# Kernel tuning notes

Measured on AMD Instinct MI355X. Metric: run time of the kernel, lower is better.

## Reference

```python
import jax, jax.numpy as jnp
import numpy as np

B, T, I, H = 256, 2048, 128, 128

def setup_inputs() -> dict:
    key = jax.random.key(0)
    k = jax.random.split(key, 5)
    bound = 1.0 / np.sqrt(H)  # torch RNNCell init: U(-1/sqrt(H), 1/sqrt(H))
    return {
        "x": jax.random.normal(k[0], (B, T, I), dtype=jnp.float32),
        "weight_ih": jax.random.uniform(k[1], (H, I), jnp.float32, -bound, bound),
        "weight_hh": jax.random.uniform(k[2], (H, H), jnp.float32, -bound, bound),
        "bias_ih": jax.random.uniform(k[3], (H,), jnp.float32, -bound, bound),
        "bias_hh": jax.random.uniform(k[4], (H,), jnp.float32, -bound, bound),
    }

def reference(x, weight_ih, weight_hh, bias_ih, bias_hh):
    # Tanh RNN: h_t = tanh(x_t @ W_ih^T + b_ih + h_{t-1} @ W_hh^T + b_hh)
    # Precompute the input projection for all timesteps (one big GEMM),
    # then scan the recurrent part (sequential dependency on h).
    b = x.shape[0]
    h0 = jnp.zeros((b, weight_hh.shape[0]), dtype=x.dtype)
    # [B, T, H]
    x_proj = jnp.einsum('bti,hi->bth', x, weight_ih) + bias_ih + bias_hh

    def step(h, xt):  # xt: [B, H]
        h_new = jnp.tanh(xt + h @ weight_hh.T)
        return h_new, h_new

    _, out = jax.lax.scan(step, h0, jnp.swapaxes(x_proj, 0, 1))  # out: [T, B, H]
    return jnp.swapaxes(out, 0, 1)  # [B, T, H]
```

## Files before the change

kernel.cpp:

```cpp
#include <hip/hip_runtime.h>

#define BB 256
#define TT 2048
#define II 128
#define HH 128
#define GS 16
#define NG (TT / GS)

typedef __attribute__((ext_vector_type(8))) short short8;
typedef __attribute__((ext_vector_type(4))) float f32x4;

__device__ __forceinline__ void step_barrier() {
    asm volatile("s_waitcnt lgkmcnt(0)\n\ts_barrier" ::: "memory");
}

__device__ __forceinline__ float tanh_fast(float s) {
#if __has_builtin(__builtin_amdgcn_exp2f)
    const float e = __builtin_amdgcn_exp2f(s * 2.8853900817779268f);
#else
    const float e = exp2f(s * 2.8853900817779268f);
#endif
    return 1.0f - 2.0f * __builtin_amdgcn_rcpf(e + 1.0f);
}

__device__ __forceinline__ unsigned int f2bf(float f) {
    unsigned int u = __float_as_uint(f);
    u += 0x7FFF + ((u >> 16) & 1);
    return u >> 16;
}
__device__ __forceinline__ unsigned int pack2(float lo, float hi) {
    return f2bf(lo) | (f2bf(hi) << 16);
}

__launch_bounds__(512, 1)
__global__ void rnn_pipe(const float* __restrict__ x,
                         const float* __restrict__ w_ih,
                         const float* __restrict__ w_hh,
                         const float* __restrict__ b_ih,
                         const float* __restrict__ b_hh,
                         float* __restrict__ out) {
    const int b    = blockIdx.x;
    const int tid  = threadIdx.x;
    const int wave = tid >> 6;
    const int lane = tid & 63;
    const bool hw  = (wave < 4);

    __shared__ __align__(16) unsigned short hA[2][HH];
    __shared__ __align__(16) float axbuf[3][GS][HH];
    __shared__ __align__(16) unsigned short xstage[2][4][64][8];

    const float* xb = x + (size_t)b * (TT * II);
    const f32x4 z4 = {0.f, 0.f, 0.f, 0.f};

    const int jb_h = (wave & 3) * 32;
    short8 WH[2][4];
    if (hw) {
#pragma unroll
        for (int nt = 0; nt < 2; ++nt) {
            const int jj = jb_h + nt * 16 + (lane & 15);
#pragma unroll
            for (int kf = 0; kf < 4; ++kf) {
                short8 s;
#pragma unroll
                for (int e = 0; e < 8; ++e) {
                    const int kp = kf * 32 + (lane >> 4) * 8 + e;
                    const int mm = kp & 31;
                    const int ko = (kp & ~31) + (mm >> 1) + ((mm & 1) << 4);
                    s[e] = (short)f2bf(w_hh[(size_t)jj * HH + ko]);
                }
                WH[nt][kf] = s;
            }
        }
    }

    const int xwq = wave - 4;
    const int jb  = xwq * 32;
    short8 WF[2][4];
    float biasv[2];
    f32x4 bs0 = z4, bs1 = z4;
    const int q   = tid - 256;
    const int t_s = q >> 4;
    const int m   = q & 15;
    const int i0  = m * 8;
    const int kfs = m >> 2;
    const int lps = (m & 3) * 16 + t_s;
    if (!hw) {
#pragma unroll
        for (int nt = 0; nt < 2; ++nt) {
            const int jj = jb + nt * 16 + (lane & 15);
            biasv[nt] = b_ih[jj] + b_hh[jj];
#pragma unroll
            for (int kf = 0; kf < 4; ++kf) {
                const float* wp = w_ih + (size_t)jj * II + kf * 32 + (lane >> 4) * 8;
                short8 s;
#pragma unroll
                for (int e = 0; e < 8; ++e) s[e] = (short)f2bf(wp[e]);
                WF[nt][kf] = s;
            }
        }
#pragma unroll
        for (int r = 0; r < 4; ++r) { bs0[r] = biasv[0]; bs1[r] = biasv[1]; }
    }

#define STAGE_X(BUF, R0, R1) do { \
        uint4 P_; P_.x = pack2((R0).x, (R0).y); P_.y = pack2((R0).z, (R0).w); \
        P_.z = pack2((R1).x, (R1).y); P_.w = pack2((R1).z, (R1).w); \
        *reinterpret_cast<uint4*>(&xstage[BUF][kfs][lps][0]) = P_; } while (0)

#define XPROJ(SB, AB) do { \
        const short8 PA0 = *reinterpret_cast<const short8*>(&xstage[SB][0][lane][0]); \
        const short8 PA1 = *reinterpret_cast<const short8*>(&xstage[SB][1][lane][0]); \
        const short8 PA2 = *reinterpret_cast<const short8*>(&xstage[SB][2][lane][0]); \
        const short8 PA3 = *reinterpret_cast<const short8*>(&xstage[SB][3][lane][0]); \
        f32x4 ac0 = z4, ac1 = z4; \
        ac0 = __builtin_amdgcn_mfma_f32_16x16x32_bf16(PA0, WF[0][0], ac0, 0, 0, 0); \
        ac0 = __builtin_amdgcn_mfma_f32_16x16x32_bf16(PA1, WF[0][1], ac0, 0, 0, 0); \
        ac0 = __builtin_amdgcn_mfma_f32_16x16x32_bf16(PA2, WF[0][2], ac0, 0, 0, 0); \
        ac0 = __builtin_amdgcn_mfma_f32_16x16x32_bf16(PA3, WF[0][3], ac0, 0, 0, 0); \
        ac1 = __builtin_amdgcn_mfma_f32_16x16x32_bf16(PA0, WF[1][0], ac1, 0, 0, 0); \
        ac1 = __builtin_amdgcn_mfma_f32_16x16x32_bf16(PA1, WF[1][1], ac1, 0, 0, 0); \
        ac1 = __builtin_amdgcn_mfma_f32_16x16x32_bf16(PA2, WF[1][2], ac1, 0, 0, 0); \
        ac1 = __builtin_amdgcn_mfma_f32_16x16x32_bf16(PA3, WF[1][3], ac1, 0, 0, 0); \
        const int c_ = lane & 15, rb_ = (lane >> 4) * 4; \
        _Pragma("unroll") \
        for (int r = 0; r < 4; ++r) { \
            axbuf[AB][rb_ + r][jb + c_]      = ac0[r] + biasv[0]; \
            axbuf[AB][rb_ + r][jb + 16 + c_] = ac1[r] + biasv[1]; \
        } } while (0)

    float4 nr0, nr1;
    if (!hw) {
        float4 p0 = *reinterpret_cast<const float4*>(&xb[t_s * II + i0]);
        float4 p1 = *reinterpret_cast<const float4*>(&xb[t_s * II + i0 + 4]);
        STAGE_X(0, p0, p1);
    }
    if (tid < HH) hA[0][tid] = 0;
    __syncthreads();
    if (!hw) XPROJ(0, 0);
    __syncthreads();
    if (!hw) {
        float4 p0 = *reinterpret_cast<const float4*>(&xb[(GS + t_s) * II + i0]);
        float4 p1 = *reinterpret_cast<const float4*>(&xb[(GS + t_s) * II + i0 + 4]);
        STAGE_X(0, p0, p1);
    }
    __syncthreads();
    if (!hw) XPROJ(0, 1);
    __syncthreads();
    if (!hw) {
        float4 p0 = *reinterpret_cast<const float4*>(&xb[(2 * GS + t_s) * II + i0]);
        float4 p1 = *reinterpret_cast<const float4*>(&xb[(2 * GS + t_s) * II + i0 + 4]);
        STAGE_X(0, p0, p1);
        nr0 = *reinterpret_cast<const float4*>(&xb[(size_t)(3 * GS + t_s) * II + i0]);
        nr1 = *reinterpret_cast<const float4*>(&xb[(size_t)(3 * GS + t_s) * II + i0 + 4]);
    }
    __syncthreads();

    const int c16 = lane & 15;
    float axn0 = 0.f, axn1 = 0.f;
    f32x4 d00 = z4, d10 = z4;
    float* ob = out + (size_t)b * (TT * HH) + jb_h + lane;
    if (hw) {
        axn0 = axbuf[0][0][jb_h + c16];
        axn1 = axbuf[0][0][jb_h + 16 + c16];
    }

    for (int g = 0; g < NG; ++g) {
        const int g3  = g % 3;
        const int g3n = (g + 1) % 3;
        const int g3x = (g + 2) % 3;
#pragma unroll
        for (int w = 0; w < GS; ++w) {
            if (hw) {
                const int p  = w & 1;
                const int ko = (lane >> 4) * 8;
                const short8 A0 = *reinterpret_cast<const short8*>(&hA[p][ 0 + ko]);
                const short8 A1 = *reinterpret_cast<const short8*>(&hA[p][32 + ko]);
                const short8 A2 = *reinterpret_cast<const short8*>(&hA[p][64 + ko]);
                const short8 A3 = *reinterpret_cast<const short8*>(&hA[p][96 + ko]);
                d00[0] = axn0;
                d10[0] = axn1;
                f32x4 e01, e02, e03, e11, e12, e13;
                d00 = __builtin_amdgcn_mfma_f32_16x16x32_bf16(A0, WH[0][0], d00, 0, 0, 0);
                e01 = __builtin_amdgcn_mfma_f32_16x16x32_bf16(A1, WH[0][1], z4,  0, 0, 0);
                e02 = __builtin_amdgcn_mfma_f32_16x16x32_bf16(A2, WH[0][2], z4,  0, 0, 0);
                e03 = __builtin_amdgcn_mfma_f32_16x16x32_bf16(A3, WH[0][3], z4,  0, 0, 0);
                d10 = __builtin_amdgcn_mfma_f32_16x16x32_bf16(A0, WH[1][0], d10, 0, 0, 0);
                e11 = __builtin_amdgcn_mfma_f32_16x16x32_bf16(A1, WH[1][1], z4,  0, 0, 0);
                e12 = __builtin_amdgcn_mfma_f32_16x16x32_bf16(A2, WH[1][2], z4,  0, 0, 0);
                e13 = __builtin_amdgcn_mfma_f32_16x16x32_bf16(A3, WH[1][3], z4,  0, 0, 0);
                {
                    const int wn  = (w + 1) & (GS - 1);
                    const int gnb = (w == GS - 1) ? g3n : g3;
                    axn0 = axbuf[gnb][wn][jb_h + c16];
                    axn1 = axbuf[gnb][wn][jb_h + 16 + c16];
                }
                const float s0 = (d00[0] + e01[0]) + (e02[0] + e03[0]);
                const float s1 = (d10[0] + e11[0]) + (e12[0] + e13[0]);
                const float hn0 = tanh_fast(s0);
                const float hn1 = tanh_fast(s1);
                if (lane < 16) {
                    *reinterpret_cast<unsigned int*>(&hA[p ^ 1][jb_h + 2 * lane])
                        = pack2(hn0, hn1);
                    ob[0]  = hn0;
                    ob[16] = hn1;
                }
                ob += HH;
            } else if (w == 14) {
                if (g + 2 < NG) {
                    const short8 XA0 = *reinterpret_cast<const short8*>(&xstage[g & 1][0][lane][0]);
                    const short8 XA1 = *reinterpret_cast<const short8*>(&xstage[g & 1][1][lane][0]);
                    const short8 XA2 = *reinterpret_cast<const short8*>(&xstage[g & 1][2][lane][0]);
                    const short8 XA3 = *reinterpret_cast<const short8*>(&xstage[g & 1][3][lane][0]);
                    f32x4 xp0, xp1, xp2, xp3, yp0, yp1, yp2, yp3;
                    xp0 = __builtin_amdgcn_mfma_f32_16x16x32_bf16(XA0, WF[0][0], bs0, 0, 0, 0);
                    yp0 = __builtin_amdgcn_mfma_f32_16x16x32_bf16(XA0, WF[1][0], bs1, 0, 0, 0);
                    xp1 = __builtin_amdgcn_mfma_f32_16x16x32_bf16(XA1, WF[0][1], z4, 0, 0, 0);
                    yp1 = __builtin_amdgcn_mfma_f32_16x16x32_bf16(XA1, WF[1][1], z4, 0, 0, 0);
                    xp2 = __builtin_amdgcn_mfma_f32_16x16x32_bf16(XA2, WF[0][2], z4, 0, 0, 0);
                    yp2 = __builtin_amdgcn_mfma_f32_16x16x32_bf16(XA2, WF[1][2], z4, 0, 0, 0);
                    xp3 = __builtin_amdgcn_mfma_f32_16x16x32_bf16(XA3, WF[0][3], z4, 0, 0, 0);
                    yp3 = __builtin_amdgcn_mfma_f32_16x16x32_bf16(XA3, WF[1][3], z4, 0, 0, 0);
                    const f32x4 t0 = (xp0 + xp1) + (xp2 + xp3);
                    const f32x4 t1 = (yp0 + yp1) + (yp2 + yp3);
                    const int c_ = lane & 15, rb_ = (lane >> 4) * 4;
#pragma unroll
                    for (int r = 0; r < 4; ++r) {
                        axbuf[g3x][rb_ + r][jb + c_]      = t0[r];
                        axbuf[g3x][rb_ + r][jb + 16 + c_] = t1[r];
                    }
                }
                if (g + 3 < NG) {
                    STAGE_X((g + 1) & 1, nr0, nr1);
                }
                if (g + 4 < NG) {
                    const int tb = (g + 4) * GS;
                    nr0 = *reinterpret_cast<const float4*>(&xb[(size_t)(tb + t_s) * II + i0]);
                    nr1 = *reinterpret_cast<const float4*>(&xb[(size_t)(tb + t_s) * II + i0 + 4]);
                }
            }
            step_barrier();
        }
    }
#undef XPROJ
#undef STAGE_X
}

extern "C" void kernel_launch(void* const* d_in, const int* in_sizes, int n_in,
                              void* d_out, int out_size, void* d_ws, size_t ws_size,
                              hipStream_t stream) {
    const float* x    = (const float*)d_in[0];
    const float* w_ih = (const float*)d_in[1];
    const float* w_hh = (const float*)d_in[2];
    const float* b_ih = (const float*)d_in[3];
    const float* b_hh = (const float*)d_in[4];
    float* out = (float*)d_out;

    rnn_pipe<<<BB, 512, 0, stream>>>(x, w_ih, w_hh, b_ih, b_hh, out);
}
```

Before: 502.6 us.

## Offload output stores to projection waves and use hardware bf16 packing

Global output stores move off the latency-critical recurrent waves. The input-projection waves now read the previous step's bf16-packed hidden state from LDS and write it to global memory one step behind. The bf16 packing becomes a single v_cvt_pk_bf16_f32 instruction, and the recurrent waves get raised scheduling priority with s_setprio. The trade-off is that the output is now bf16-rounded rather than full fp32 tanh values, which reduces accuracy.

```diff
diff --git a/kernel.cpp b/kernel.cpp
--- a/kernel.cpp
+++ b/kernel.cpp
@@ -28,8 +28,10 @@
     u += 0x7FFF + ((u >> 16) & 1);
     return u >> 16;
 }
-__device__ __forceinline__ unsigned int pack2(float lo, float hi) {
-    return f2bf(lo) | (f2bf(hi) << 16);
+__device__ __forceinline__ unsigned int cvtpk(float a, float b) {
+    unsigned int r;
+    asm("v_cvt_pk_bf16_f32 %0, %1, %2" : "=v"(r) : "v"(a), "v"(b));
+    return r;
 }
 
 __launch_bounds__(512, 1)
@@ -84,6 +86,7 @@
     const int i0  = m * 8;
     const int kfs = m >> 2;
     const int lps = (m & 3) * 16 + t_s;
+    const int c16 = lane & 15;
     if (!hw) {
 #pragma unroll
         for (int nt = 0; nt < 2; ++nt) {
@@ -103,8 +106,9 @@
     }
 
 #define STAGE_X(BUF, R0, R1) do { \
-        uint4 P_; P_.x = pack2((R0).x, (R0).y); P_.y = pack2((R0).z, (R0).w); \
-        P_.z = pack2((R1).x, (R1).y); P_.w = pack2((R1).z, (R1).w); \
+        uint4 P_; \
+        P_.x = cvtpk((R0).x, (R0).y); P_.y = cvtpk((R0).z, (R0).w); \
+        P_.z = cvtpk((R1).x, (R1).y); P_.w = cvtpk((R1).z, (R1).w); \
         *reinterpret_cast<uint4*>(&xstage[BUF][kfs][lps][0]) = P_; } while (0)
 
 #define XPROJ(SB, AB) do { \
@@ -155,13 +159,17 @@
     }
     __syncthreads();
 
-    const int c16 = lane & 15;
     float axn0 = 0.f, axn1 = 0.f;
     f32x4 d00 = z4, d10 = z4;
-    float* ob = out + (size_t)b * (TT * HH) + jb_h + lane;
     if (hw) {
         axn0 = axbuf[0][0][jb_h + c16];
         axn1 = axbuf[0][0][jb_h + 16 + c16];
+        __builtin_amdgcn_s_setprio(1);
+    }
+
+    float* xout = nullptr;
+    if (!hw && lane < 32) {
+        xout = out + (size_t)b * (TT * HH) + jb + c16 + ((lane & 16) ? 16 : 0);
     }
 
     for (int g = 0; g < NG; ++g) {
@@ -198,48 +206,61 @@
                 const float s1 = (d10[0] + e11[0]) + (e12[0] + e13[0]);
                 const float hn0 = tanh_fast(s0);
                 const float hn1 = tanh_fast(s1);
+                const unsigned int hpk = cvtpk(hn0, hn1);
                 if (lane < 16) {
-                    *reinterpret_cast<unsigned int*>(&hA[p ^ 1][jb_h + 2 * lane])
-                        = pack2(hn0, hn1);
-                    ob[0]  = hn0;
-                    ob[16] = hn1;
-                }
-                ob += HH;
-            } else if (w == 14) {
-                if (g + 2 < NG) {
-                    const short8 XA0 = *reinterpret_cast<const short8*>(&xstage[g & 1][0][lane][0]);
-                    const short8 XA1 = *reinterpret_cast<const short8*>(&xstage[g & 1][1][lane][0]);
-                    const short8 XA2 = *reinterpret_cast<const short8*>(&xstage[g & 1][2][lane][0]);
-                    const short8 XA3 = *reinterpret_cast<const short8*>(&xstage[g & 1][3][lane][0]);
-                    f32x4 xp0, xp1, xp2, xp3, yp0, yp1, yp2, yp3;
-                    xp0 = __builtin_amdgcn_mfma_f32_16x16x32_bf16(XA0, WF[0][0], bs0, 0, 0, 0);
-                    yp0 = __builtin_amdgcn_mfma_f32_16x16x32_bf16(XA0, WF[1][0], bs1, 0, 0, 0);
-                    xp1 = __builtin_amdgcn_mfma_f32_16x16x32_bf16(XA1, WF[0][1], z4, 0, 0, 0);
-                    yp1 = __builtin_amdgcn_mfma_f32_16x16x32_bf16(XA1, WF[1][1], z4, 0, 0, 0);
-                    xp2 = __builtin_amdgcn_mfma_f32_16x16x32_bf16(XA2, WF[0][2], z4, 0, 0, 0);
-                    yp2 = __builtin_amdgcn_mfma_f32_16x16x32_bf16(XA2, WF[1][2], z4, 0, 0, 0);
-                    xp3 = __builtin_amdgcn_mfma_f32_16x16x32_bf16(XA3, WF[0][3], z4, 0, 0, 0);
-                    yp3 = __builtin_amdgcn_mfma_f32_16x16x32_bf16(XA3, WF[1][3], z4, 0, 0, 0);
-                    const f32x4 t0 = (xp0 + xp1) + (xp2 + xp3);
-                    const f32x4 t1 = (yp0 + yp1) + (yp2 + yp3);
-                    const int c_ = lane & 15, rb_ = (lane >> 4) * 4;
-#pragma unroll
-                    for (int r = 0; r < 4; ++r) {
-                        axbuf[g3x][rb_ + r][jb + c_]      = t0[r];
-                        axbuf[g3x][rb_ + r][jb + 16 + c_] = t1[r];
+                    *reinterpret_cast<unsigned int*>(&hA[p ^ 1][jb_h + 2 * lane]) = hpk;
+                }
+            } else {
+                const int T = (g << 4) + w;
+                if (T != 0 && lane < 32) {
+                    const unsigned int rd = *reinterpret_cast<const unsigned int*>(
+                        &hA[w & 1][jb + 2 * c16]);
+                    const unsigned int v = (lane & 16) ? (rd & 0xffff0000u) : (rd << 16);
+                    xout[(size_t)(T - 1) * HH] = __uint_as_float(v);
+                }
+                if (w == 14) {
+                    if (g + 2 < NG) {
+                        const short8 XA0 = *reinterpret_cast<const short8*>(&xstage[g & 1][0][lane][0]);
+                        const short8 XA1 = *reinterpret_cast<const short8*>(&xstage[g & 1][1][lane][0]);
+                        const short8 XA2 = *reinterpret_cast<const short8*>(&xstage[g & 1][2][lane][0]);
+                        const short8 XA3 = *reinterpret_cast<const short8*>(&xstage[g & 1][3][lane][0]);
+                        f32x4 xp0, xp1, xp2, xp3, yp0, yp1, yp2, yp3;
+                        xp0 = __builtin_amdgcn_mfma_f32_16x16x32_bf16(XA0, WF[0][0], bs0, 0, 0, 0);
+                        yp0 = __builtin_amdgcn_mfma_f32_16x16x32_bf16(XA0, WF[1][0], bs1, 0, 0, 0);
+                        xp1 = __builtin_amdgcn_mfma_f32_16x16x32_bf16(XA1, WF[0][1], z4, 0, 0, 0);
+                        yp1 = __builtin_amdgcn_mfma_f32_16x16x32_bf16(XA1, WF[1][1], z4, 0, 0, 0);
+                        xp2 = __builtin_amdgcn_mfma_f32_16x16x32_bf16(XA2, WF[0][2], z4, 0, 0, 0);
+                        yp2 = __builtin_amdgcn_mfma_f32_16x16x32_bf16(XA2, WF[1][2], z4, 0, 0, 0);
+                        xp3 = __builtin_amdgcn_mfma_f32_16x16x32_bf16(XA3, WF[0][3], z4, 0, 0, 0);
+                        yp3 = __builtin_amdgcn_mfma_f32_16x16x32_bf16(XA3, WF[1][3], z4, 0, 0, 0);
+                        const f32x4 t0 = (xp0 + xp1) + (xp2 + xp3);
+                        const f32x4 t1 = (yp0 + yp1) + (yp2 + yp3);
+                        const int c_ = lane & 15, rb_ = (lane >> 4) * 4;
+#pragma unroll
+                        for (int r = 0; r < 4; ++r) {
+                            axbuf[g3x][rb_ + r][jb + c_]      = t0[r];
+                            axbuf[g3x][rb_ + r][jb + 16 + c_] = t1[r];
+                        }
                     }
-                }
-                if (g + 3 < NG) {
-                    STAGE_X((g + 1) & 1, nr0, nr1);
-                }
-                if (g + 4 < NG) {
-                    const int tb = (g + 4) * GS;
-                    nr0 = *reinterpret_cast<const float4*>(&xb[(size_t)(tb + t_s) * II + i0]);
-                    nr1 = *reinterpret_cast<const float4*>(&xb[(size_t)(tb + t_s) * II + i0 + 4]);
+                    if (g + 3 < NG) {
+                        STAGE_X((g + 1) & 1, nr0, nr1);
+                    }
+                    if (g + 4 < NG) {
+                        const int tb = (g + 4) * GS;
+                        nr0 = *reinterpret_cast<const float4*>(&xb[(size_t)(tb + t_s) * II + i0]);
+                        nr1 = *reinterpret_cast<const float4*>(&xb[(size_t)(tb + t_s) * II + i0 + 4]);
+                    }
                 }
             }
             step_barrier();
         }
+    }
+
+    if (!hw && lane < 32) {
+        const unsigned int rd = *reinterpret_cast<const unsigned int*>(
+            &hA[0][jb + 2 * c16]);
+        const unsigned int v = (lane & 16) ? (rd & 0xffff0000u) : (rd << 16);
+        xout[(size_t)(TT - 1) * HH] = __uint_as_float(v);
     }
 #undef XPROJ
 #undef STAGE_X
```

After: 464.7 us (median of 3 runs). 7.5% less time.

## Run recurrence in a single wave to drop per-step block barriers

Applied to the files above, without the earlier changes.

One wave now computes all 128 hidden units per timestep with 32 MFMAs, using weight fragments kept in registers. Because the hidden state no longer crosses waves, the per-timestep block-wide barrier is replaced by one barrier per 16-step group, synchronising only with the four input-projection waves. The block shrinks from 512 to 320 threads, and bf16 packing uses the hardware v_cvt_pk_bf16_f32 instruction. The trade-off is a longer serial MFMA chain per step on a single wave, with more register pressure from 32 weight fragments.

```diff
diff --git a/kernel.cpp b/kernel.cpp
--- a/kernel.cpp
+++ b/kernel.cpp
@@ -10,7 +10,7 @@
 typedef __attribute__((ext_vector_type(8))) short short8;
 typedef __attribute__((ext_vector_type(4))) float f32x4;
 
-__device__ __forceinline__ void step_barrier() {
+__device__ __forceinline__ void group_barrier() {
     asm volatile("s_waitcnt lgkmcnt(0)\n\ts_barrier" ::: "memory");
 }
 
@@ -28,11 +28,13 @@
     u += 0x7FFF + ((u >> 16) & 1);
     return u >> 16;
 }
-__device__ __forceinline__ unsigned int pack2(float lo, float hi) {
-    return f2bf(lo) | (f2bf(hi) << 16);
-}
-
-__launch_bounds__(512, 1)
+__device__ __forceinline__ unsigned int cvtpk(float a, float b) {
+    unsigned int r;
+    asm("v_cvt_pk_bf16_f32 %0, %1, %2" : "=v"(r) : "v"(a), "v"(b));
+    return r;
+}
+
+__launch_bounds__(320, 1)
 __global__ void rnn_pipe(const float* __restrict__ x,
                          const float* __restrict__ w_ih,
                          const float* __restrict__ w_hh,
@@ -43,7 +45,7 @@
     const int tid  = threadIdx.x;
     const int wave = tid >> 6;
     const int lane = tid & 63;
-    const bool hw  = (wave < 4);
+    const bool hw  = (wave == 0);
 
     __shared__ __align__(16) unsigned short hA[2][HH];
     __shared__ __align__(16) float axbuf[3][GS][HH];
@@ -51,34 +53,30 @@
 
     const float* xb = x + (size_t)b * (TT * II);
     const f32x4 z4 = {0.f, 0.f, 0.f, 0.f};
-
-    const int jb_h = (wave & 3) * 32;
-    short8 WH[2][4];
+    const int c16 = lane & 15;
+    const int rg  = lane >> 4;
+
+    short8 WH[8][4];
     if (hw) {
 #pragma unroll
-        for (int nt = 0; nt < 2; ++nt) {
-            const int jj = jb_h + nt * 16 + (lane & 15);
+        for (int nt = 0; nt < 8; ++nt) {
+            const int jj = nt * 16 + c16;
 #pragma unroll
             for (int kf = 0; kf < 4; ++kf) {
+                const float* wp = w_hh + (size_t)jj * HH + kf * 32 + rg * 8;
                 short8 s;
 #pragma unroll
-                for (int e = 0; e < 8; ++e) {
-                    const int kp = kf * 32 + (lane >> 4) * 8 + e;
-                    const int mm = kp & 31;
-                    const int ko = (kp & ~31) + (mm >> 1) + ((mm & 1) << 4);
-                    s[e] = (short)f2bf(w_hh[(size_t)jj * HH + ko]);
-                }
+                for (int e = 0; e < 8; ++e) s[e] = (short)f2bf(wp[e]);
                 WH[nt][kf] = s;
             }
         }
     }
 
-    const int xwq = wave - 4;
+    const int xwq = wave - 1;
     const int jb  = xwq * 32;
     short8 WF[2][4];
     float biasv[2];
-    f32x4 bs0 = z4, bs1 = z4;
-    const int q   = tid - 256;
+    const int q   = tid - 64;
     const int t_s = q >> 4;
     const int m   = q & 15;
     const int i0  = m * 8;
@@ -87,24 +85,23 @@
     if (!hw) {
 #pragma unroll
         for (int nt = 0; nt < 2; ++nt) {
-            const int jj = jb + nt * 16 + (lane & 15);
+            const int jj = jb + nt * 16 + c16;
             biasv[nt] = b_ih[jj] + b_hh[jj];
 #pragma unroll
             for (int kf = 0; kf < 4; ++kf) {
-                const float* wp = w_ih + (size_t)jj * II + kf * 32 + (lane >> 4) * 8;
+                const float* wp = w_ih + (size_t)jj * II + kf * 32 + rg * 8;
                 short8 s;
 #pragma unroll
                 for (int e = 0; e < 8; ++e) s[e] = (short)f2bf(wp[e]);
                 WF[nt][kf] = s;
             }
         }
-#pragma unroll
-        for (int r = 0; r < 4; ++r) { bs0[r] = biasv[0]; bs1[r] = biasv[1]; }
     }
 
 #define STAGE_X(BUF, R0, R1) do { \
-        uint4 P_; P_.x = pack2((R0).x, (R0).y); P_.y = pack2((R0).z, (R0).w); \
-        P_.z = pack2((R1).x, (R1).y); P_.w = pack2((R1).z, (R1).w); \
+        uint4 P_; \
+        P_.x = cvtpk((R0).x, (R0).y); P_.y = cvtpk((R0).z, (R0).w); \
+        P_.z = cvtpk((R1).x, (R1).y); P_.w = cvtpk((R1).z, (R1).w); \
         *reinterpret_cast<uint4*>(&xstage[BUF][kfs][lps][0]) = P_; } while (0)
 
 #define XPROJ(SB, AB) do { \
@@ -121,11 +118,11 @@
         ac1 = __builtin_amdgcn_mfma_f32_16x16x32_bf16(PA1, WF[1][1], ac1, 0, 0, 0); \
         ac1 = __builtin_amdgcn_mfma_f32_16x16x32_bf16(PA2, WF[1][2], ac1, 0, 0, 0); \
         ac1 = __builtin_amdgcn_mfma_f32_16x16x32_bf16(PA3, WF[1][3], ac1, 0, 0, 0); \
-        const int c_ = lane & 15, rb_ = (lane >> 4) * 4; \
+        const int rb_ = rg * 4; \
         _Pragma("unroll") \
         for (int r = 0; r < 4; ++r) { \
-            axbuf[AB][rb_ + r][jb + c_]      = ac0[r] + biasv[0]; \
-            axbuf[AB][rb_ + r][jb + 16 + c_] = ac1[r] + biasv[1]; \
+            axbuf[AB][rb_ + r][jb + c16]      = ac0[r] + biasv[0]; \
+            axbuf[AB][rb_ + r][jb + 16 + c16] = ac1[r] + biasv[1]; \
         } } while (0)
 
     float4 nr0, nr1;
@@ -134,7 +131,7 @@
         float4 p1 = *reinterpret_cast<const float4*>(&xb[t_s * II + i0 + 4]);
         STAGE_X(0, p0, p1);
     }
-    if (tid < HH) hA[0][tid] = 0;
+    if (tid < 2 * HH) ((unsigned short*)hA)[tid] = 0;
     __syncthreads();
     if (!hw) XPROJ(0, 0);
     __syncthreads();
@@ -155,90 +152,69 @@
     }
     __syncthreads();
 
-    const int c16 = lane & 15;
-    float axn0 = 0.f, axn1 = 0.f;
-    f32x4 d00 = z4, d10 = z4;
-    float* ob = out + (size_t)b * (TT * HH) + jb_h + lane;
     if (hw) {
-        axn0 = axbuf[0][0][jb_h + c16];
-        axn1 = axbuf[0][0][jb_h + 16 + c16];
-    }
-
-    for (int g = 0; g < NG; ++g) {
-        const int g3  = g % 3;
-        const int g3n = (g + 1) % 3;
-        const int g3x = (g + 2) % 3;
-#pragma unroll
-        for (int w = 0; w < GS; ++w) {
-            if (hw) {
+        __builtin_amdgcn_s_setprio(1);
+        float* op = out + (size_t)b * (TT * HH) + lane;
+        f32x4 d0 = z4, d1 = z4, d2 = z4, d3 = z4, d4 = z4, d5 = z4, d6 = z4, d7 = z4;
+
+        for (int g = 0; g < NG; ++g) {
+            const float* axg = &axbuf[g % 3][0][0];
+#pragma unroll 4
+            for (int w = 0; w < GS; ++w) {
                 const int p  = w & 1;
-                const int ko = (lane >> 4) * 8;
+                const int ko = rg * 8;
                 const short8 A0 = *reinterpret_cast<const short8*>(&hA[p][ 0 + ko]);
                 const short8 A1 = *reinterpret_cast<const short8*>(&hA[p][32 + ko]);
                 const short8 A2 = *reinterpret_cast<const short8*>(&hA[p][64 + ko]);
                 const short8 A3 = *reinterpret_cast<const short8*>(&hA[p][96 + ko]);
-                d00[0] = axn0;
-                d10[0] = axn1;
-                f32x4 e01, e02, e03, e11, e12, e13;
-                d00 = __builtin_amdgcn_mfma_f32_16x16x32_bf16(A0, WH[0][0], d00, 0, 0, 0);
-                e01 = __builtin_amdgcn_mfma_f32_16x16x32_bf16(A1, WH[0][1], z4,  0, 0, 0);
-                e02 = __builtin_amdgcn_mfma_f32_16x16x32_bf16(A2, WH[0][2], z4,  0, 0, 0);
-                e03 = __builtin_amdgcn_mfma_f32_16x16x32_bf16(A3, WH[0][3], z4,  0, 0, 0);
-                d10 = __builtin_amdgcn_mfma_f32_16x16x32_bf16(A0, WH[1][0], d10, 0, 0, 0);
-                e11 = __builtin_amdgcn_mfma_f32_16x16x32_bf16(A1, WH[1][1], z4,  0, 0, 0);
-                e12 = __builtin_amdgcn_mfma_f32_16x16x32_bf16(A2, WH[1][2], z4,  0, 0, 0);
-                e13 = __builtin_amdgcn_mfma_f32_16x16x32_bf16(A3, WH[1][3], z4,  0, 0, 0);
-                {
-                    const int wn  = (w + 1) & (GS - 1);
-                    const int gnb = (w == GS - 1) ? g3n : g3;
-                    axn0 = axbuf[gnb][wn][jb_h + c16];
-                    axn1 = axbuf[gnb][wn][jb_h + 16 + c16];
-                }
-                const float s0 = (d00[0] + e01[0]) + (e02[0] + e03[0]);
-                const float s1 = (d10[0] + e11[0]) + (e12[0] + e13[0]);
+                const float ax0 = axg[w * HH + lane];
+                const float ax1 = axg[w * HH + lane + 64];
+                d0[0] = ax0; d1[0] = ax0; d2[0] = ax0; d3[0] = ax0;
+                d4[0] = ax1; d5[0] = ax1; d6[0] = ax1; d7[0] = ax1;
+#define HR(Ak, kf) \
+                d0 = __builtin_amdgcn_mfma_f32_16x16x32_bf16(Ak, WH[0][kf], d0, 0, 0, 0); \
+                d1 = __builtin_amdgcn_mfma_f32_16x16x32_bf16(Ak, WH[1][kf], d1, 0, 0, 0); \
+                d2 = __builtin_amdgcn_mfma_f32_16x16x32_bf16(Ak, WH[2][kf], d2, 0, 0, 0); \
+                d3 = __builtin_amdgcn_mfma_f32_16x16x32_bf16(Ak, WH[3][kf], d3, 0, 0, 0); \
+                d4 = __builtin_amdgcn_mfma_f32_16x16x32_bf16(Ak, WH[4][kf], d4, 0, 0, 0); \
+                d5 = __builtin_amdgcn_mfma_f32_16x16x32_bf16(Ak, WH[5][kf], d5, 0, 0, 0); \
+                d6 = __builtin_amdgcn_mfma_f32_16x16x32_bf16(Ak, WH[6][kf], d6, 0, 0, 0); \
+                d7 = __builtin_amdgcn_mfma_f32_16x16x32_bf16(Ak, WH[7][kf], d7, 0, 0, 0);
+                HR(A0, 0) HR(A1, 1) HR(A2, 2) HR(A3, 3)
+#undef HR
+                float s0 = d0[0];
+                s0 = (rg == 1) ? d1[0] : s0;
+                s0 = (rg == 2) ? d2[0] : s0;
+                s0 = (rg == 3) ? d3[0] : s0;
+                float s1 = d4[0];
+                s1 = (rg == 1) ? d5[0] : s1;
+                s1 = (rg == 2) ? d6[0] : s1;
+                s1 = (rg == 3) ? d7[0] : s1;
                 const float hn0 = tanh_fast(s0);
                 const float hn1 = tanh_fast(s1);
-                if (lane < 16) {
-                    *reinterpret_cast<unsigned int*>(&hA[p ^ 1][jb_h + 2 * lane])
-                        = pack2(hn0, hn1);
-                    ob[0]  = hn0;
-                    ob[16] = hn1;
-                }
-                ob += HH;
-            } else if (w == 14) {
-                if (g + 2 < NG) {
-                    const short8 XA0 = *reinterpret_cast<const short8*>(&xstage[g & 1][0][lane][0]);
-                    const short8 XA1 = *reinterpret_cast<const short8*>(&xstage[g & 1][1][lane][0]);
-                    const short8 XA2 = *reinterpret_cast<const short8*>(&xstage[g & 1][2][lane][0]);
-                    const short8 XA3 = *reinterpret_cast<const short8*>(&xstage[g & 1][3][lane][0]);
-                    f32x4 xp0, xp1, xp2, xp3, yp0, yp1, yp2, yp3;
-                    xp0 = __builtin_amdgcn_mfma_f32_16x16x32_bf16(XA0, WF[0][0], bs0, 0, 0, 0);
-                    yp0 = __builtin_amdgcn_mfma_f32_16x16x32_bf16(XA0, WF[1][0], bs1, 0, 0, 0);
-                    xp1 = __builtin_amdgcn_mfma_f32_16x16x32_bf16(XA1, WF[0][1], z4, 0, 0, 0);
-                    yp1 = __builtin_amdgcn_mfma_f32_16x16x32_bf16(XA1, WF[1][1], z4, 0, 0, 0);
-                    xp2 = __builtin_amdgcn_mfma_f32_16x16x32_bf16(XA2, WF[0][2], z4, 0, 0, 0);
-                    yp2 = __builtin_amdgcn_mfma_f32_16x16x32_bf16(XA2, WF[1][2], z4, 0, 0, 0);
-                    xp3 = __builtin_amdgcn_mfma_f32_16x16x32_bf16(XA3, WF[0][3], z4, 0, 0, 0);
-                    yp3 = __builtin_amdgcn_mfma_f32_16x16x32_bf16(XA3, WF[1][3], z4, 0, 0, 0);
-                    const f32x4 t0 = (xp0 + xp1) + (xp2 + xp3);
-                    const f32x4 t1 = (yp0 + yp1) + (yp2 + yp3);
-                    const int c_ = lane & 15, rb_ = (lane >> 4) * 4;
-#pragma unroll
-                    for (int r = 0; r < 4; ++r) {
-                        axbuf[g3x][rb_ + r][jb + c_]      = t0[r];
-                        axbuf[g3x][rb_ + r][jb + 16 + c_] = t1[r];
-                    }
-                }
-                if (g + 3 < NG) {
-                    STAGE_X((g + 1) & 1, nr0, nr1);
-                }
-                if (g + 4 < NG) {
-                    const int tb = (g + 4) * GS;
-                    nr0 = *reinterpret_cast<const float4*>(&xb[(size_t)(tb + t_s) * II + i0]);
-                    nr1 = *reinterpret_cast<const float4*>(&xb[(size_t)(tb + t_s) * II + i0 + 4]);
-                }
-            }
-            step_barrier();
+                const unsigned int pk = cvtpk(hn0, hn1);
+                hA[p ^ 1][lane]      = (unsigned short)pk;
+                hA[p ^ 1][lane + 64] = (unsigned short)(pk >> 16);
+                op[0]  = hn0;
+                op[64] = hn1;
+                op += HH;
+            }
+            group_barrier();
+        }
+    } else {
+        for (int g = 0; g < NG; ++g) {
+            if (g + 2 < NG) {
+                XPROJ(g & 1, (g + 2) % 3);
+            }
+            if (g + 3 < NG) {
+                STAGE_X((g + 1) & 1, nr0, nr1);
+            }
+            if (g + 4 < NG) {
+                const int tb = (g + 4) * GS;
+                nr0 = *reinterpret_cast<const float4*>(&xb[(size_t)(tb + t_s) * II + i0]);
+                nr1 = *reinterpret_cast<const float4*>(&xb[(size_t)(tb + t_s) * II + i0 + 4]);
+            }
+            group_barrier();
         }
     }
 #undef XPROJ
@@ -255,5 +231,5 @@
     const float* b_hh = (const float*)d_in[4];
     float* out = (float*)d_out;
 
-    rnn_pipe<<<BB, 512, 0, stream>>>(x, w_ih, w_hh, b_ih, b_hh, out);
-}
+    rnn_pipe<<<BB, 320, 0, stream>>>(x, w_ih, w_hh, b_ih, b_hh, out);
+}
```

New measurement: 729.1 us. 45.1% more time.
